# Optimization experiments

Measured on AMD Instinct MI355X. Metric: run time of the kernel, lower is better.

The kernel has to match this reference:

```python
import jax, jax.numpy as jnp
import numpy as np

NEG = 0.2  # LeakyReLU slope

def lrelu(x):
    return jnp.where(x >= 0, x, NEG * x)

def conv2d(x, w, pad):
    return jax.lax.conv_general_dilated(x, w, (1, 1), [(pad, pad), (pad, pad)],
                                        dimension_numbers=('NCHW', 'OIHW', 'NCHW'))

def maxpool2(x):
    return jax.lax.reduce_window(x, -jnp.inf, jax.lax.max, (1, 1, 2, 2), (1, 1, 2, 2), 'VALID')

def batchnorm(x, g, b, eps=1e-5):
    m = jnp.mean(x, axis=(0, 2, 3), keepdims=True)
    v = jnp.var(x, axis=(0, 2, 3), keepdims=True)
    return (x - m) / jnp.sqrt(v + eps) * g[None, :, None, None] + b[None, :, None, None]

def features(x, cw1, bg1, bb1, cw2, bg2, bb2, cw3, bg3, bb3, cw4, bg4, bb4):
    x = maxpool2(lrelu(batchnorm(conv2d(x, cw1, 1), bg1, bb1)))
    x = maxpool2(lrelu(batchnorm(conv2d(x, cw2, 1), bg2, bb2)))
    x = lrelu(batchnorm(conv2d(x, cw3, 1), bg3, bb3))
    x = lrelu(batchnorm(conv2d(x, cw4, 1), bg4, bb4))
    return x  # [B,64,16,16]

def mhsa(x, wq, bq, wk, bk, wv, bv, rel_h, rel_w, ln_g, ln_b, heads=4):
    B, C, W, H = x.shape
    d, hw = C // heads, W * H
    def proj(w, b):
        return (jnp.einsum('oc,bchw->bohw', w, x) + b[None, :, None, None]).reshape(B, heads, d, hw)
    q, k, v = proj(wq, bq), proj(wk, bk), proj(wv, bv)
    cc = jnp.einsum('bhdi,bhdj->bhij', q, k)                 # content-content
    pos = (rel_h + rel_w).reshape(heads, d, hw)              # relative position bias
    cp = jnp.einsum('hdi,bhdj->bhij', pos, q)                # content-position
    attn = jax.nn.softmax(cc + cp, axis=-1)
    out = jnp.einsum('bhdj,bhij->bhdi', v, attn).reshape(B, C, W, H)
    m = jnp.mean(out, axis=(1, 2, 3), keepdims=True)
    va = jnp.var(out, axis=(1, 2, 3), keepdims=True)
    out = (out - m) / jnp.sqrt(va + 1e-5) * ln_g[None] + ln_b[None]
    return out + x

def cbam(x, cw1, cb1, cw2, cb2, sw, sb):
    avg, mx = jnp.mean(x, axis=(2, 3)), jnp.max(x, axis=(2, 3))
    def exc(f):
        return jnp.einsum('oc,bc->bo', cw2, jax.nn.relu(jnp.einsum('oc,bc->bo', cw1, f) + cb1)) + cb2
    x = jax.nn.sigmoid(exc(avg) + exc(mx))[:, :, None, None] * x
    sf = jnp.stack([jnp.mean(x, axis=1), jnp.max(x, axis=1)], axis=1)  # [B,2,H,W]
    sa = jax.nn.sigmoid(conv2d(sf, sw, 3) + sb[None, :, None, None])
    return sa * x

def sa_module(x, mh, cb):
    return mhsa(x, *mh) + cbam(x, *cb) + x

def setup_inputs() -> dict:
    key = jax.random.key(0)
    ks = jax.random.split(key, 24)
    rn = lambda k, s, sc=1.0: jax.random.normal(k, s, dtype=jnp.float32) * sc
    inp = {
        'input1': rn(ks[0], (64, 1, 64, 64)),
        'input2': rn(ks[1], (5, 5, 1, 64, 64)),
        'conv1_w': rn(ks[2], (64, 1, 3, 3), 0.3),
        'bn1_g': jnp.ones(64), 'bn1_b': jnp.zeros(64),
        'conv2_w': rn(ks[3], (64, 64, 3, 3), 0.05),
        'bn2_g': jnp.ones(64), 'bn2_b': jnp.zeros(64),
        'conv3_w': rn(ks[4], (64, 64, 3, 3), 0.05),
        'bn3_g': jnp.ones(64), 'bn3_b': jnp.zeros(64),
        'conv4_w': rn(ks[5], (64, 64, 3, 3), 0.05),
        'bn4_g': jnp.ones(64), 'bn4_b': jnp.zeros(64),
        'wq': rn(ks[6], (64, 64), 0.12), 'bq': rn(ks[7], (64,), 0.01),
        'wk': rn(ks[8], (64, 64), 0.12), 'bk': rn(ks[9], (64,), 0.01),
        'wv': rn(ks[10], (64, 64), 0.12), 'bv': rn(ks[11], (64,), 0.01),
        'rel_h': rn(ks[12], (1, 4, 16, 1, 16)),
        'rel_w': rn(ks[13], (1, 4, 16, 16, 1)),
        'ln_g': jnp.ones((64, 16, 16)), 'ln_b': jnp.zeros((64, 16, 16)),
        'ca_w1': rn(ks[14], (4, 64), 0.15), 'ca_b1': jnp.zeros(4),
        'ca_w2': rn(ks[15], (64, 4), 0.15), 'ca_b2': jnp.zeros(64),
        'sa_w': rn(ks[16], (1, 2, 7, 7), 0.1), 'sa_b': jnp.zeros(1),
        'cls_w': rn(ks[17], (256,), 0.05),
    }
    return inp

def reference(input1, input2, conv1_w, bn1_g, bn1_b, conv2_w, bn2_g, bn2_b,
              conv3_w, bn3_g, bn3_b, conv4_w, bn4_g, bn4_b,
              wq, bq, wk, bk, wv, bv, rel_h, rel_w, ln_g, ln_b,
              ca_w1, ca_b1, ca_w2, ca_b2, sa_w, sa_b, cls_w):
    fa = (conv1_w, bn1_g, bn1_b, conv2_w, bn2_g, bn2_b, conv3_w, bn3_g, bn3_b, conv4_w, bn4_g, bn4_b)
    mh = (wq, bq, wk, bk, wv, bv, rel_h, rel_w, ln_g, ln_b)
    cb = (ca_w1, ca_b1, ca_w2, ca_b2, sa_w, sa_b)
    q = sa_module(features(input1, *fa), mh, cb)                      # [B,64,16,16]
    S = jax.vmap(lambda imgs: sa_module(features(imgs, *fa), mh, cb))(input2)  # [ncls,shot,64,16,16]
    ncls, shot = input2.shape[0], input2.shape[1]
    B, C, Hh, Ww = q.shape
    hw = Hh * Ww
    # per-class covariance over channels (CovaBlock.cal_covariance)
    X = S.transpose(0, 2, 1, 3, 4).reshape(ncls, C, shot * hw)
    Xc = X - jnp.mean(X, axis=2, keepdims=True)
    cov = jnp.einsum('ncm,ndm->ncd', Xc, Xc) / (hw * shot - 1)        # [ncls,C,C]
    # query similarity: diag(q^T Cov q) done as fused quadratic form
    Q = q.reshape(B, C, hw)
    Qn = Q / jnp.linalg.norm(Q, axis=2, keepdims=True)
    sim = jnp.einsum('bci,jcd,bdi->bji', Qn, cov, Qn)                 # [B,ncls,hw]
    # classifier: LeakyReLU -> Dropout(eval=identity) -> Conv1d(k=hw, stride=hw, no bias)
    out = jnp.einsum('bjk,k->bj', lrelu(sim), cls_w)
    return out
```

## Files before the change

kernel.cpp:

```cpp
#include <hip/hip_runtime.h>
#include <hip/hip_bf16.h>

__device__ __forceinline__ float lrelu(float x){ return x >= 0.f ? x : 0.2f*x; }
__device__ __forceinline__ float sigm(float x){ return 1.f/(1.f+__expf(-x)); }

typedef short short8 __attribute__((ext_vector_type(8)));
typedef float f32x16 __attribute__((ext_vector_type(16)));

static constexpr size_t OFF_X0    = 0;
static constexpr size_t OFF_POS   = 475712;
static constexpr size_t OFF_WQT   = 492096;
static constexpr size_t OFF_STATS = 504384;
static constexpr size_t OFF_P1    = 507456;
static constexpr size_t OFF_P2    = 6340160;
static constexpr size_t OFF_RES   = 10714688;
static constexpr size_t OFF_MU    = 12172864;
static constexpr size_t OFF_COV   = 12173184;
static constexpr size_t OFF_SIM   = 12193664;
static constexpr size_t OFF_R1    = 12275584;
static constexpr size_t OFF_C2    = OFF_R1;
static constexpr size_t OFF_ATP   = OFF_R1;
static constexpr size_t OFF_C3    = OFF_R1 + 5832704;
static constexpr size_t OFF_C4    = OFF_R1 + 8749056;
static constexpr size_t OFF_CKV   = OFF_R1 + 10207232;
static constexpr size_t OFF_MHRAW = OFF_R1 + 14581760;
static constexpr size_t OFF_QN    = OFF_R1 + 17543680;
static constexpr size_t OFF_WH    = OFF_R1 + 21737984;
static constexpr size_t OFF_WL    = OFF_WH + 18432;

__device__ __forceinline__ int bn_group(int img){ return (img < 64) ? 0 : (1 + (img-64)/5); }

__device__ __forceinline__ void bn_ab(const float* __restrict__ sums, int g, int c, float n,
                                      float gw, float bw, float& a, float& b)
{
    const float sum = sums[(g*64+c)*2], ss = sums[(g*64+c)*2+1];
    const float m = sum/n;
    const float var = fmaxf(ss/n - m*m, 0.f);
    const float istd = 1.f/sqrtf(var + 1e-5f);
    a = gw*istd;
    b = bw - m*a;
}

__global__ __launch_bounds__(256) void prep_k(const float* __restrict__ in1, const float* __restrict__ in2,
        const float* __restrict__ relh, const float* __restrict__ relw,
        const float* __restrict__ wq, const float* __restrict__ wk, const float* __restrict__ wv,
        const float* __restrict__ cw2,
        float* __restrict__ ws)
{
    int idx = blockIdx.x*256 + threadIdx.x;
    if (idx < 364544) { ws[OFF_X0+idx] = (idx < 262144 ? in1[idx] : in2[idx-262144]); return; }
    idx -= 364544;
    if (idx < 16384) {
        const int h = idx>>12, r = idx&4095, i = r>>4, d = r&15;
        ws[OFF_POS+idx] = relh[h*256 + d*16 + (i&15)] + relw[h*256 + d*16 + (i>>4)];
        return;
    }
    idx -= 16384;
    if (idx < 12288) {
        const int s = idx/4096, r = idx%4096, c = r>>6, o = r&63;
        const float* wp = (s==0)?wq:((s==1)?wk:wv);
        ws[OFF_WQT+idx] = wp[o*64 + c];
        return;
    }
    idx -= 12288;
    if (idx < 3072) { ws[OFF_STATS+idx] = 0.f; return; }
    idx -= 3072;
    if (idx < 20480) { ws[OFF_COV+idx] = 0.f; return; }
    idx -= 20480;
    if (idx < 36864) {
        const int och = idx/576, r = idx%576, cin = r/9, k9 = r%9;
        const float v = cw2[idx];
        __hip_bfloat16 hb = __float2bfloat16(v);
        const float hv = __bfloat162float(hb);
        __hip_bfloat16 lb = __float2bfloat16(v - hv);
        unsigned short* WH = (unsigned short*)(ws + OFF_WH);
        unsigned short* WL = (unsigned short*)(ws + OFF_WL);
        const int d = k9*4096 + och*64 + cin;
        WH[d] = *(unsigned short*)&hb;
        WL[d] = *(unsigned short*)&lb;
    }
}

template<int H, int W, int CIN, int CH, int OCB, int PT, bool STORE, bool INBN>
__global__ __launch_bounds__(256) void conv3x3_k(const float* __restrict__ in,
                                                 const float* __restrict__ wt,
                                                 float* __restrict__ out,
                                                 float* __restrict__ bnsum,
                                                 const float* __restrict__ isums,
                                                 const float* __restrict__ igw,
                                                 const float* __restrict__ ibw,
                                                 int ihw)
{
    constexpr int P = W + 1;
    constexpr int PLANE = H * P;
    constexpr int HW = H * W;
    constexpr int PASSES = HW / (256 * PT);
    constexpr int NLD = CH * HW / 256;
    __shared__ float lds[CH * PLANE];
    __shared__ float redS[OCB*4], redQ[OCB*4];
    __shared__ float abA[64], abB[64];
    const int img = blockIdx.x;
    const int och0 = blockIdx.y * OCB;
    const int t = threadIdx.x;

    if constexpr (INBN) {
        if (t < CIN) {
            const int gi = bn_group(img);
            const float nin = (float)(((gi==0)?64:5) * ihw);
            float a, b;
            bn_ab(isums, gi, t, nin, igw[t], ibw[t], a, b);
            abA[t]=a; abB[t]=b;
        }
        __syncthreads();
    }

    float acc[PASSES][OCB][PT];
#pragma unroll
    for (int a=0;a<PASSES;a++)
#pragma unroll
      for (int o=0;o<OCB;o++)
#pragma unroll
        for (int p=0;p<PT;p++) acc[a][o][p]=0.f;

    for (int idx = t; idx < CH*HW; idx += 256) {
        const int c = idx / HW, p = idx % HW;
        float v = in[((size_t)img*CIN + c)*HW + p];
        if constexpr (INBN) v = lrelu(abA[c]*v + abB[c]);
        lds[c*PLANE + (p/W)*P + (p%W)] = v;
    }
    __syncthreads();

    for (int cc0 = 0; cc0 < CIN; cc0 += CH) {
        float pre[(CIN > CH) ? NLD : 1];
        if constexpr (CIN > CH) {
            if (cc0 + CH < CIN) {
#pragma unroll
                for (int j=0;j<NLD;j++){
                    const int idx = j*256 + t;
                    const int c = idx / HW, p = idx % HW;
                    pre[j] = in[((size_t)img*CIN + cc0 + CH + c)*HW + p];
                }
            }
        }
        for (int c = 0; c < CH; ++c) {
            float wr[OCB][9];
#pragma unroll
            for (int o=0;o<OCB;o++)
#pragma unroll
              for (int k=0;k<9;k++)
                wr[o][k] = wt[((size_t)(och0+o)*CIN + (cc0+c))*9 + k];
            const float* Lc = lds + c*PLANE;
#pragma unroll
            for (int ps=0; ps<PASSES; ++ps) {
                const int px0 = (ps*256 + t)*PT;
                const int y = px0 / W, x0 = px0 % W;
#pragma unroll
                for (int ky=0; ky<3; ++ky) {
                    const int yy = y + ky - 1;
                    if (yy >= 0 && yy < H) {
                        const float* Lr = Lc + yy*P;
                        float r[PT+2];
                        r[0] = (x0 > 0) ? Lr[x0-1] : 0.f;
#pragma unroll
                        for (int k2=0;k2<PT;k2++) r[k2+1] = Lr[x0+k2];
                        r[PT+1] = (x0+PT < W) ? Lr[x0+PT] : 0.f;
#pragma unroll
                        for (int p=0;p<PT;p++)
#pragma unroll
                          for (int kx=0;kx<3;kx++) {
                              const float v = r[p+kx];
#pragma unroll
                              for (int o=0;o<OCB;o++)
                                  acc[ps][o][p] += v * wr[o][ky*3+kx];
                          }
                    }
                }
            }
        }
        if constexpr (CIN > CH) {
            if (cc0 + CH < CIN) {
                __syncthreads();
#pragma unroll
                for (int j=0;j<NLD;j++){
                    const int idx = j*256 + t;
                    const int c = idx / HW, p = idx % HW;
                    float v = pre[j];
                    if constexpr (INBN) v = lrelu(abA[cc0+CH+c]*v + abB[cc0+CH+c]);
                    lds[c*PLANE + (p/W)*P + (p%W)] = v;
                }
                __syncthreads();
            }
        }
    }
    if constexpr (STORE) {
#pragma unroll
        for (int ps=0; ps<PASSES; ++ps) {
            const int px0 = (ps*256 + t)*PT;
#pragma unroll
            for (int o=0;o<OCB;o++)
#pragma unroll
              for (int p=0;p<PT;p++)
                out[((size_t)img*64 + och0+o)*HW + px0 + p] = acc[ps][o][p];
        }
    }
    const int g = bn_group(img);
    const int wv = t >> 6;
#pragma unroll
    for (int o=0;o<OCB;o++){
        float s=0.f, ss=0.f;
#pragma unroll
        for (int ps=0;ps<PASSES;ps++)
#pragma unroll
          for (int p=0;p<PT;p++){ const float v=acc[ps][o][p]; s+=v; ss+=v*v; }
#pragma unroll
        for (int off=32; off>0; off>>=1){ s += __shfl_xor(s, off); ss += __shfl_xor(ss, off); }
        if ((t&63)==0){ redS[o*4+wv]=s; redQ[o*4+wv]=ss; }
    }
    __syncthreads();
    if (t < OCB*2){
        const int o = t>>1, metric = t&1;
        const float v = metric ? (redQ[o*4]+redQ[o*4+1]+redQ[o*4+2]+redQ[o*4+3])
                               : (redS[o*4]+redS[o*4+1]+redS[o*4+2]+redS[o*4+3]);
        atomicAdd(&bnsum[(g*64 + och0+o)*2 + metric], v);
    }
}

__global__ __launch_bounds__(256) void conv2mfma_k(const float* __restrict__ p1,
        const unsigned short* __restrict__ whi, const unsigned short* __restrict__ wlo,
        float* __restrict__ c2)
{
    __shared__ __align__(16) unsigned short Bx[6*34*72];
    const int img = blockIdx.x, rowblk = blockIdx.y;
    const int t = threadIdx.x;

    for (int i=t; i<6*2*72; i+=256){
        const int ly = i/144, r2 = i%144, xs = r2/72, c = r2%72;
        Bx[(ly*34 + xs*33)*72 + c] = 0;
    }
    unsigned int lo_pack[24];
    const int y0 = rowblk*4 - 1;
    {
        int it = 0;
        for (int lin=t; lin<12288; lin+=256, ++it){
            const int c = lin/192, r = lin%192, ly = r>>5, x = r&31;
            const int y = y0 + ly;
            float v = 0.f;
            if (y>=0 && y<32) v = p1[((size_t)img*64 + c)*1024 + y*32 + x];
            __hip_bfloat16 hb = __float2bfloat16(v);
            const float hv = __bfloat162float(hb);
            __hip_bfloat16 lb = __float2bfloat16(v - hv);
            Bx[(ly*34 + x + 1)*72 + c] = *(unsigned short*)&hb;
            const unsigned int lu = *(unsigned short*)&lb;
            if (it & 1) lo_pack[it>>1] |= (lu<<16); else lo_pack[it>>1] = lu;
        }
    }
    __syncthreads();

    const int lane = t & 63, wv = t >> 6;
    const int mt = wv & 1, ntp = wv >> 1;
    const int m = lane & 31, kg = lane >> 5;
    const int nt0 = ntp*2, nt1 = nt0 + 1;

    f32x16 acc0, acc1;
#pragma unroll
    for (int r=0;r<16;r++){ acc0[r]=0.f; acc1[r]=0.f; }

    for (int ky=0; ky<3; ky++){
      for (int kx=0; kx<3; kx++){
        const int s = ky*3 + kx;
        const unsigned short* wh = whi + ((s*64 + mt*32 + m)<<6) + kg*8;
        const unsigned short* wl = wlo + ((s*64 + mt*32 + m)<<6) + kg*8;
        const int b0 = ((nt0+ky)*34 + m + kx)*72 + kg*8;
        const int b1 = ((nt1+ky)*34 + m + kx)*72 + kg*8;
        short8 ah[4], al[4], bh0[4], bh1[4];
#pragma unroll
        for (int ch=0; ch<4; ch++){
            ah[ch]  = *(const short8*)(wh + ch*16);
            al[ch]  = *(const short8*)(wl + ch*16);
            bh0[ch] = *(const short8*)(Bx + b0 + ch*16);
            bh1[ch] = *(const short8*)(Bx + b1 + ch*16);
        }
#pragma unroll
        for (int ch=0; ch<4; ch++){
            acc0 = __builtin_amdgcn_mfma_f32_32x32x16_bf16(ah[ch], bh0[ch], acc0, 0,0,0);
            acc1 = __builtin_amdgcn_mfma_f32_32x32x16_bf16(ah[ch], bh1[ch], acc1, 0,0,0);
        }
#pragma unroll
        for (int ch=0; ch<4; ch++){
            acc0 = __builtin_amdgcn_mfma_f32_32x32x16_bf16(al[ch], bh0[ch], acc0, 0,0,0);
            acc1 = __builtin_amdgcn_mfma_f32_32x32x16_bf16(al[ch], bh1[ch], acc1, 0,0,0);
        }
      }
    }
    __syncthreads();
    {
        int it = 0;
        for (int lin=t; lin<12288; lin+=256, ++it){
            const int c = lin/192, r = lin%192, ly = r>>5, x = r&31;
            const unsigned int lu = (it&1) ? (lo_pack[it>>1]>>16) : (lo_pack[it>>1]&0xffffu);
            Bx[(ly*34 + x + 1)*72 + c] = (unsigned short)lu;
        }
    }
    __syncthreads();
    for (int ky=0; ky<3; ky++){
      for (int kx=0; kx<3; kx++){
        const int s = ky*3 + kx;
        const unsigned short* wh = whi + ((s*64 + mt*32 + m)<<6) + kg*8;
        const int b0 = ((nt0+ky)*34 + m + kx)*72 + kg*8;
        const int b1 = ((nt1+ky)*34 + m + kx)*72 + kg*8;
#pragma unroll
        for (int ch=0; ch<4; ch++){
            const short8 ah  = *(const short8*)(wh + ch*16);
            const short8 bl0 = *(const short8*)(Bx + b0 + ch*16);
            const short8 bl1 = *(const short8*)(Bx + b1 + ch*16);
            acc0 = __builtin_amdgcn_mfma_f32_32x32x16_bf16(ah, bl0, acc0, 0,0,0);
            acc1 = __builtin_amdgcn_mfma_f32_32x32x16_bf16(ah, bl1, acc1, 0,0,0);
        }
      }
    }
    const int px0 = (rowblk*4 + nt0)*32 + m;
    const int px1 = (rowblk*4 + nt1)*32 + m;
#pragma unroll
    for (int r=0; r<16; r++){
        const int och = mt*32 + (r&3) + 8*(r>>2) + 4*kg;
        c2[((size_t)img*64 + och)*1024 + px0] = acc0[r];
        c2[((size_t)img*64 + och)*1024 + px1] = acc1[r];
    }
}

__global__ __launch_bounds__(256) void bnstats2_k(const float* __restrict__ in, float* __restrict__ sums)
{
    __shared__ float rs[4], rq[4];
    const int img = blockIdx.x, c = blockIdx.y, t = threadIdx.x;
    const float4 v = ((const float4*)(in + ((size_t)img*64 + c)*1024))[t];
    float s = v.x+v.y+v.z+v.w;
    float q = v.x*v.x+v.y*v.y+v.z*v.z+v.w*v.w;
#pragma unroll
    for (int off=32; off>0; off>>=1){ s += __shfl_xor(s, off); q += __shfl_xor(q, off); }
    if ((t&63)==0){ rs[t>>6]=s; rq[t>>6]=q; }
    __syncthreads();
    if (t==0){
        const int g = bn_group(img);
        atomicAdd(&sums[(g*64+c)*2],   rs[0]+rs[1]+rs[2]+rs[3]);
        atomicAdd(&sums[(g*64+c)*2+1], rq[0]+rq[1]+rq[2]+rq[3]);
    }
}

__global__ __launch_bounds__(256) void bnpoolconv1_k(const float* __restrict__ x0,
        const float* __restrict__ cw, const float* __restrict__ sums,
        const float* __restrict__ gw, const float* __restrict__ bw,
        float* __restrict__ out)
{
    __shared__ float xl[64*65];
    const int img = blockIdx.x, och = blockIdx.y, t = threadIdx.x;
    const float* xp = x0 + (size_t)img*4096;
    for (int idx=t; idx<4096; idx+=256) xl[(idx>>6)*65 + (idx&63)] = xp[idx];
    float w[9];
#pragma unroll
    for (int k=0;k<9;k++) w[k] = cw[och*9+k];
    const int g = bn_group(img);
    const float n = (float)(((g==0)?64:5) * 4096);
    float a, b;
    bn_ab(sums, g, och, n, gw[och], bw[och], a, b);
    __syncthreads();
    const int oy = t>>3, ox0 = (t&7)*4;
    float r[4][10];
#pragma unroll
    for (int rr=0; rr<4; ++rr){
        const int yy = 2*oy-1+rr;
#pragma unroll
        for (int cc=0; cc<10; ++cc){
            const int xx = 2*ox0-1+cc;
            r[rr][cc] = (yy>=0 && yy<64 && xx>=0 && xx<64) ? xl[yy*65+xx] : 0.f;
        }
    }
    float4 res;
    float* rp = (float*)&res;
#pragma unroll
    for (int p=0;p<4;p++){
        float best = -1e30f;
#pragma unroll
        for (int sy=0; sy<2; ++sy)
#pragma unroll
          for (int sx=0; sx<2; ++sx){
            float s=0.f;
#pragma unroll
            for (int ky=0;ky<3;ky++)
#pragma unroll
              for (int kx=0;kx<3;kx++)
                s += r[sy+ky][2*p+sx+kx]*w[ky*3+kx];
            best = fmaxf(best, lrelu(a*s+b));
          }
        rp[p] = best;
    }
    *(float4*)(out + ((size_t)img*64+och)*1024 + oy*32 + ox0) = res;
}

template<int H, int W>
__global__ __launch_bounds__(256) void bnpool_k(const float* __restrict__ in, const float* __restrict__ sums,
                                 const float* __restrict__ gw, const float* __restrict__ bw,
                                 float* __restrict__ out)
{
    const int img = blockIdx.x, c = blockIdx.y, t = threadIdx.x;
    const int g = bn_group(img);
    const float n = (float)(((g==0)?64:5) * H * W);
    float a, b;
    bn_ab(sums, g, c, n, gw[c], bw[c], a, b);
    constexpr int W2=W/2, HW=H*W, N2=(H/2)*W2;
    const float* pl = in + ((size_t)img*64 + c)*HW;
    float* po = out + ((size_t)img*64 + c)*N2;
    for (int opx=t; opx<N2; opx+=256) {
        const int oy=opx/W2, ox=opx%W2;
        const float* q = pl + (2*oy)*W + 2*ox;
        const float v0=lrelu(a*q[0]+b), v1=lrelu(a*q[1]+b), v2=lrelu(a*q[W]+b), v3=lrelu(a*q[W+1]+b);
        po[opx] = fmaxf(fmaxf(v0,v1),fmaxf(v2,v3));
    }
}

__global__ __launch_bounds__(256) void proj_k(const float* __restrict__ c4, const float* __restrict__ wT,
               const float* __restrict__ bq, const float* __restrict__ bk, const float* __restrict__ bv,
               const float* __restrict__ sums4, const float* __restrict__ gw4, const float* __restrict__ bw4,
               float* __restrict__ ckv)
{
    __shared__ float xl[64*256];
    const int img = blockIdx.x, s = blockIdx.y, t = threadIdx.x;
    const int gi = bn_group(img);
    const float nin = (float)(((gi==0)?64:5) * 256);
    {
        const float4* in4 = (const float4*)(c4 + (size_t)img*16384);
        float4* xl4 = (float4*)xl;
        for (int i=t; i<4096; i+=256){
            float4 v = in4[i];
            const int c = i>>6;
            float a, b;
            bn_ab(sums4, gi, c, nin, gw4[c], bw4[c], a, b);
            v.x=lrelu(a*v.x+b); v.y=lrelu(a*v.y+b); v.z=lrelu(a*v.z+b); v.w=lrelu(a*v.w+b);
            xl4[i] = v;
        }
    }
    const float* bias = (s==0)?bq:((s==1)?bk:bv);
    const int sofs = (s==0)?16:((s==1)?0:32);
    const float* wp = wT + s*4096;
    const int o0 = (t>>4)*4, i0 = (t&15)*16;
    const int h = o0>>4, d0 = o0&15;
    __syncthreads();
    float acc[4][16];
    float b0[4];
#pragma unroll
    for (int o=0;o<4;o++) b0[o]=bias[o0+o];
#pragma unroll
    for (int o=0;o<4;o++)
#pragma unroll
      for (int i=0;i<16;i++) acc[o][i]=b0[o];
    for (int c=0;c<64;c++){
        const float4 w4 = *(const float4*)(wp + c*64 + o0);
        const float* xr = xl + c*256 + i0;
#pragma unroll
        for (int k=0;k<4;k++){
            const float4 x4 = *(const float4*)(xr + 4*k);
            acc[0][4*k+0]+=w4.x*x4.x; acc[0][4*k+1]+=w4.x*x4.y; acc[0][4*k+2]+=w4.x*x4.z; acc[0][4*k+3]+=w4.x*x4.w;
            acc[1][4*k+0]+=w4.y*x4.x; acc[1][4*k+1]+=w4.y*x4.y; acc[1][4*k+2]+=w4.y*x4.z; acc[1][4*k+3]+=w4.y*x4.w;
            acc[2][4*k+0]+=w4.z*x4.x; acc[2][4*k+1]+=w4.z*x4.y; acc[2][4*k+2]+=w4.z*x4.z; acc[2][4*k+3]+=w4.z*x4.w;
            acc[3][4*k+0]+=w4.w*x4.x; acc[3][4*k+1]+=w4.w*x4.y; acc[3][4*k+2]+=w4.w*x4.z; acc[3][4*k+3]+=w4.w*x4.w;
        }
    }
#pragma unroll
    for (int ii=0;ii<16;ii++){
        const float4 v = make_float4(acc[0][ii],acc[1][ii],acc[2][ii],acc[3][ii]);
        *(float4*)(ckv + (((size_t)img*4 + h)*256 + i0+ii)*48 + sofs + d0) = v;
    }
}

__global__ __launch_bounds__(256) void attnp_k(const float* __restrict__ ckv, const float* __restrict__ pos,
                               float* __restrict__ part)
{
    const int img = blockIdx.x, h = blockIdx.y, jc = blockIdx.z, i = threadIdx.x;
    const size_t jb = (((size_t)img*4 + h)*256)*48;
    float areg[32];
    {
        const float* myrow = ckv + jb + (size_t)i*48;
#pragma unroll
        for (int k=0;k<4;k++) *(float4*)&areg[4*k]    = *(const float4*)(myrow + 16 + 4*k);
#pragma unroll
        for (int k=0;k<4;k++) *(float4*)&areg[16+4*k] = *(const float4*)(pos + h*4096 + i*16 + 4*k);
    }
    float mrun = -1e30f, l = 0.f;
    float accv[16];
#pragma unroll
    for (int d=0;d<16;d++) accv[d]=0.f;

    const int jend = jc*64 + 64;
    for (int j0=jc*64; j0<jend; j0+=2){
        const float* r0 = ckv + jb + (size_t)j0*48;
        const float* r1 = r0 + 48;
        float s0a=0.f, s0b=0.f, s1a=0.f, s1b=0.f;
#pragma unroll
        for (int dd=0; dd<16; ++dd){
            s0a += areg[2*dd]  *r0[2*dd];
            s0b += areg[2*dd+1]*r0[2*dd+1];
            s1a += areg[2*dd]  *r1[2*dd];
            s1b += areg[2*dd+1]*r1[2*dd+1];
        }
        const float s0 = s0a+s0b, s1 = s1a+s1b;
        const float mnew = fmaxf(mrun, fmaxf(s0,s1));
        const float al = __expf(mrun - mnew);
        const float e0 = __expf(s0 - mnew), e1 = __expf(s1 - mnew);
        mrun = mnew;
        l = l*al + e0 + e1;
        const float* v0 = r0 + 32;
        const float* v1 = r1 + 32;
#pragma unroll
        for (int d=0;d<16;d++) accv[d] = accv[d]*al + e0*v0[d] + e1*v1[d];
    }
    float* pp = part + ((((size_t)img*4 + h)*4 + jc)*18)*256;
    pp[i]       = mrun;
    pp[256 + i] = l;
#pragma unroll
    for (int d=0;d<16;d++) pp[(2+d)*256 + i] = accv[d];
}

__global__ __launch_bounds__(256) void attnm_k(const float* __restrict__ part, float* __restrict__ mhraw)
{
    const int img = blockIdx.x, h = blockIdx.y, i = threadIdx.x;
    const float* pb = part + (((size_t)img*4 + h)*4*18)*256;
    float mc[4], lc[4];
#pragma unroll
    for (int c=0;c<4;c++){ mc[c] = pb[c*4608 + i]; lc[c] = pb[c*4608 + 256 + i]; }
    const float ms = fmaxf(fmaxf(mc[0],mc[1]), fmaxf(mc[2],mc[3]));
    float wgt[4]; float ls = 0.f;
#pragma unroll
    for (int c=0;c<4;c++){ wgt[c] = __expf(mc[c]-ms); ls += wgt[c]*lc[c]; }
    const float rl = 1.f/ls;
#pragma unroll
    for (int d=0;d<16;d++){
        float v = 0.f;
#pragma unroll
        for (int c=0;c<4;c++) v += wgt[c]*pb[c*4608 + (2+d)*256 + i];
        mhraw[((size_t)img*64 + h*16 + d)*256 + i] = v*rl;
    }
}

__global__ __launch_bounds__(256) void post_k(const float* __restrict__ mhraw,
        const float* __restrict__ lng, const float* __restrict__ lnb,
        const float* __restrict__ c4,
        const float* __restrict__ sums4, const float* __restrict__ gw4, const float* __restrict__ bw4,
        const float* __restrict__ w1, const float* __restrict__ b1,
        const float* __restrict__ w2, const float* __restrict__ b2,
        const float* __restrict__ sw, const float* __restrict__ sb,
        float* __restrict__ res)
{
    __shared__ float r1[256], r2[256];
    __shared__ float favg[64], fmx[64], z1s[8], ca[64];
    __shared__ float sf[512];
    __shared__ float wl[98];
    __shared__ float mh_s[2];
    __shared__ float aA[64], aB[64];
    __shared__ float sa_l[256];
    const int img = blockIdx.x, t = threadIdx.x;
    const float* mb  = mhraw + (size_t)img*16384;
    const float* fbr = c4    + (size_t)img*16384;

    if (t<64){
        const int gi = bn_group(img);
        const float nin = (float)(((gi==0)?64:5) * 256);
        float a, b;
        bn_ab(sums4, gi, t, nin, gw4[t], bw4[t], a, b);
        aA[t]=a; aB[t]=b;
    }
    if (t<98) wl[t] = sw[t];

    {
        const float4* mb4 = (const float4*)mb;
        float s=0.f, ss=0.f;
        for (int i=t; i<4096; i+=256){
            const float4 v = mb4[i];
            s  += v.x+v.y+v.z+v.w;
            ss += v.x*v.x+v.y*v.y+v.z*v.z+v.w*v.w;
        }
        r1[t]=s; r2[t]=ss; __syncthreads();
        for (int st=128;st>0;st>>=1){ if(t<st){r1[t]+=r1[t+st]; r2[t]+=r2[t+st];} __syncthreads(); }
        if (t==0){
            const float m = r1[0]/16384.f;
            const float var = fmaxf(r2[0]/16384.f - m*m, 0.f);
            mh_s[0]=m; mh_s[1]=1.f/sqrtf(var+1e-5f);
        }
    }
    {
        const int c = t>>2, part = t&3;
        const float a = aA[c], b = aB[c];
        const float4* p4 = (const float4*)(fbr + c*256 + part*64);
        float s=0.f, mx=-1e30f;
        for (int k=0;k<16;k++){
            const float4 v = p4[k];
            const float f0=lrelu(a*v.x+b), f1=lrelu(a*v.y+b), f2=lrelu(a*v.z+b), f3=lrelu(a*v.w+b);
            s += f0+f1+f2+f3;
            mx = fmaxf(mx, fmaxf(fmaxf(f0,f1),fmaxf(f2,f3)));
        }
        __syncthreads();
        r1[t]=s; r2[t]=mx;
        __syncthreads();
        if (t<64){
            favg[t] = (r1[t*4]+r1[t*4+1]+r1[t*4+2]+r1[t*4+3])/256.f;
            fmx[t]  = fmaxf(fmaxf(r2[t*4],r2[t*4+1]),fmaxf(r2[t*4+2],r2[t*4+3]));
        }
    }
    __syncthreads();
    if (t<8){
        const int which = t>>2, o = t&3;
        const float* f = which? fmx : favg;
        float z = b1[o];
        for (int c=0;c<64;c++) z += w1[o*64+c]*f[c];
        z1s[t] = fmaxf(z, 0.f);
    }
    __syncthreads();
    if (t<64){
        float z = 2.f*b2[t];
#pragma unroll
        for (int k=0;k<4;k++) z += w2[t*4+k]*(z1s[k]+z1s[4+k]);
        ca[t] = sigm(z);
    }
    __syncthreads();
    {
        float s=0.f, mx=-1e30f;
        for (int c=0;c<64;c++){
            const float fv = lrelu(aA[c]*fbr[c*256+t] + aB[c]);
            const float v = ca[c]*fv;
            s += v; mx = fmaxf(mx, v);
        }
        sf[t]     = s/64.f;
        sf[256+t] = mx;
    }
    __syncthreads();
    {
        float sacc = sb[0];
        const int y = t>>4, x = t&15;
        for (int ch=0; ch<2; ++ch)
          for (int ky=0; ky<7; ++ky){
            const int yy = y+ky-3;
            if (yy<0||yy>=16) continue;
            for (int kx=0; kx<7; ++kx){
                const int xx = x+kx-3;
                if (xx<0||xx>=16) continue;
                sacc += sf[ch*256 + yy*16 + xx]*wl[ch*49 + ky*7 + kx];
            }
          }
        sa_l[t] = sigm(sacc);
    }
    __syncthreads();
    {
        const int q = t & 63;
        const int cb = t >> 6;
        const float m = mh_s[0], istd = mh_s[1];
        const float4* mb4 = (const float4*)mb;
        const float4* fb4 = (const float4*)fbr;
        const float4* lg4 = (const float4*)lng;
        const float4* lb4 = (const float4*)lnb;
        float4* res4 = (float4*)(res + (size_t)img*16384);
        const float sa0=sa_l[4*q], sa1=sa_l[4*q+1], sa2=sa_l[4*q+2], sa3=sa_l[4*q+3];
#pragma unroll 4
        for (int cc=0; cc<16; ++cc){
            const int c = cb*16 + cc;
            const int i4 = c*64 + q;
            const float4 mv = mb4[i4], fv = fb4[i4], gv = lg4[i4], bv = lb4[i4];
            const float a = aA[c], b = aB[c], cf = ca[c];
            float4 r;
            r.x = (mv.x-m)*istd*gv.x + bv.x + lrelu(a*fv.x+b)*(2.f + sa0*cf);
            r.y = (mv.y-m)*istd*gv.y + bv.y + lrelu(a*fv.y+b)*(2.f + sa1*cf);
            r.z = (mv.z-m)*istd*gv.z + bv.z + lrelu(a*fv.z+b)*(2.f + sa2*cf);
            r.w = (mv.w-m)*istd*gv.w + bv.w + lrelu(a*fv.w+b)*(2.f + sa3*cf);
            res4[i4] = r;
        }
    }
}

__global__ __launch_bounds__(256) void covmu_k(const float* __restrict__ res, float* __restrict__ mu)
{
    __shared__ float r1[256];
    const int n = blockIdx.x, c = blockIdx.y, t = threadIdx.x;
    float s=0.f;
    for (int sh=0; sh<5; ++sh)
        s += res[((size_t)(64 + n*5 + sh)*64 + c)*256 + t];
    r1[t]=s; __syncthreads();
    for (int st=128;st>0;st>>=1){ if(t<st) r1[t]+=r1[t+st]; __syncthreads(); }
    if (t==0) mu[n*64+c] = r1[0]/1280.f;
}

__global__ __launch_bounds__(256) void cov_k(const float* __restrict__ res, const float* __restrict__ mu,
                                             float* __restrict__ cov)
{
    __shared__ float Xl[64*129];
    const int n = blockIdx.x, by = blockIdx.y, sh = blockIdx.z, t = threadIdx.x;
    const int c = by*16 + (t>>4);
    const int d0 = (t&15)*4;
    float acc[4] = {0.f,0.f,0.f,0.f};
    for (int half=0; half<2; ++half){
        __syncthreads();
        for (int idx=t; idx<8192; idx+=256){
            const int ch = idx>>7, p = idx&127;
            Xl[ch*129+p] = res[((size_t)(64+n*5+sh)*64 + ch)*256 + half*128 + p] - mu[n*64+ch];
        }
        __syncthreads();
        for (int p=0;p<128;p++){
            const float xc = Xl[c*129+p];
#pragma unroll
            for (int k=0;k<4;k++) acc[k] += xc*Xl[(d0+k)*129+p];
        }
    }
#pragma unroll
    for (int k=0;k<4;k++) atomicAdd(&cov[((size_t)n*64 + c)*64 + d0+k], acc[k]*(1.f/1279.f));
}

__global__ __launch_bounds__(64) void qn_k(const float* __restrict__ res, float* __restrict__ qn)
{
    const int b = blockIdx.x, c = blockIdx.y, t = threadIdx.x;
    const size_t base = ((size_t)b*64 + c)*256;
    const float4 v = *(const float4*)(res + base + t*4);
    float ss = v.x*v.x + v.y*v.y + v.z*v.z + v.w*v.w;
#pragma unroll
    for (int off=32; off>0; off>>=1) ss += __shfl_xor(ss, off);
    const float inv = 1.f/sqrtf(ss);
    float4 o; o.x=v.x*inv; o.y=v.y*inv; o.z=v.z*inv; o.w=v.w*inv;
    *(float4*)(qn + base + t*4) = o;
}

__global__ __launch_bounds__(256) void sim_k(const float* __restrict__ qn, const float* __restrict__ cov,
                                             float* __restrict__ sim)
{
    __shared__ float covj[64*65];
    __shared__ float Vl[64*68];
    __shared__ float simred[320];
    const int b = blockIdx.x, iq = blockIdx.y, t = threadIdx.x;
    const int i0g = iq*64;
    for (int idx=t; idx<4096; idx+=256){
        const int c = idx>>6, il = idx&63;
        Vl[c*68+il] = qn[((size_t)b*64+c)*256 + i0g + il];
    }
    for (int idx=t; idx<320; idx+=256) simred[idx]=0.f;
    const int c0 = (t>>4)*4, i0 = (t&15)*4;
    for (int j=0;j<5;j++){
        __syncthreads();
        for (int idx=t; idx<4096; idx+=256)
            covj[(idx>>6)*65 + (idx&63)] = cov[(size_t)j*4096 + idx];
        __syncthreads();
        float pt[4][4];
#pragma unroll
        for (int a=0;a<4;a++)
#pragma unroll
          for (int bb=0;bb<4;bb++) pt[a][bb]=0.f;
        for (int d=0; d<64; ++d){
            const float4 vv = *(const float4*)&Vl[d*68 + i0];
            float cw[4];
#pragma unroll
            for (int cc=0;cc<4;cc++) cw[cc] = covj[(c0+cc)*65 + d];
#pragma unroll
            for (int cc=0;cc<4;cc++){
                pt[cc][0] += cw[cc]*vv.x;
                pt[cc][1] += cw[cc]*vv.y;
                pt[cc][2] += cw[cc]*vv.z;
                pt[cc][3] += cw[cc]*vv.w;
            }
        }
#pragma unroll
        for (int ii=0;ii<4;ii++){
            float s = 0.f;
#pragma unroll
            for (int cc=0;cc<4;cc++) s += pt[cc][ii]*Vl[(c0+cc)*68 + i0+ii];
            atomicAdd(&simred[j*64 + i0 + ii], s);
        }
    }
    __syncthreads();
    for (int idx=t; idx<320; idx+=256){
        const int j = idx>>6, il = idx&63;
        sim[((size_t)b*5 + j)*256 + i0g + il] = simred[idx];
    }
}

__global__ __launch_bounds__(256) void cls_k(const float* __restrict__ sim, const float* __restrict__ cw,
                                             float* __restrict__ out)
{
    __shared__ float red[256];
    const int b = blockIdx.x, t = threadIdx.x;
    const float w = cw[t];
    for (int j=0;j<5;j++){
        const float v = sim[((size_t)b*5 + j)*256 + t];
        red[t] = lrelu(v)*w;
        __syncthreads();
        for (int st=128;st>0;st>>=1){ if(t<st) red[t]+=red[t+st]; __syncthreads(); }
        if (t==0) out[b*5+j] = red[0];
        __syncthreads();
    }
}

extern "C" void kernel_launch(void* const* d_in, const int* in_sizes, int n_in,
                              void* d_out, int out_size, void* d_ws, size_t ws_size,
                              hipStream_t stream)
{
    const float* IN[31];
    for (int i=0;i<31;i++) IN[i] = (const float*)d_in[i];
    float* W = (float*)d_ws;
    float* OUT = (float*)d_out;
    const unsigned short* WHp = (const unsigned short*)(W + OFF_WH);
    const unsigned short* WLp = (const unsigned short*)(W + OFF_WL);

    prep_k<<<1772,256,0,stream>>>(IN[0],IN[1],IN[20],IN[21],IN[14],IN[16],IN[18],IN[5],W);

    conv3x3_k<64,64,1,1,4,4,false,false><<<dim3(89,16),256,0,stream>>>(W+OFF_X0, IN[2], nullptr, W+OFF_STATS, nullptr,nullptr,nullptr,0);
    bnpoolconv1_k<<<dim3(89,64),256,0,stream>>>(W+OFF_X0, IN[2], W+OFF_STATS, IN[3], IN[4], W+OFF_P1);

    conv2mfma_k<<<dim3(89,8),256,0,stream>>>(W+OFF_P1, WHp, WLp, W+OFF_C2);
    bnstats2_k<<<dim3(89,64),256,0,stream>>>(W+OFF_C2, W+OFF_STATS+768);
    bnpool_k<32,32><<<dim3(89,64),256,0,stream>>>(W+OFF_C2, W+OFF_STATS+768, IN[6], IN[7], W+OFF_P2);

    conv3x3_k<16,16,64,16,8,1,true,false><<<dim3(89,8),256,0,stream>>>(W+OFF_P2, IN[8], W+OFF_C3, W+OFF_STATS+1536, nullptr,nullptr,nullptr,0);

    conv3x3_k<16,16,64,16,8,1,true,true><<<dim3(89,8),256,0,stream>>>(W+OFF_C3, IN[11], W+OFF_C4, W+OFF_STATS+2304,
                                                                      W+OFF_STATS+1536, IN[9], IN[10], 256);

    proj_k<<<dim3(89,3),256,0,stream>>>(W+OFF_C4, W+OFF_WQT, IN[15], IN[17], IN[19],
                                        W+OFF_STATS+2304, IN[12], IN[13], W+OFF_CKV);
    attnp_k<<<dim3(89,4,4),256,0,stream>>>(W+OFF_CKV, W+OFF_POS, W+OFF_ATP);
    attnm_k<<<dim3(89,4),256,0,stream>>>(W+OFF_ATP, W+OFF_MHRAW);

    post_k<<<89,256,0,stream>>>(W+OFF_MHRAW, IN[22], IN[23], W+OFF_C4,
                                W+OFF_STATS+2304, IN[12], IN[13],
                                IN[24], IN[25], IN[26], IN[27], IN[28], IN[29], W+OFF_RES);

    covmu_k<<<dim3(5,64),256,0,stream>>>(W+OFF_RES, W+OFF_MU);
    cov_k<<<dim3(5,4,5),256,0,stream>>>(W+OFF_RES, W+OFF_MU, W+OFF_COV);
    qn_k<<<dim3(64,64),64,0,stream>>>(W+OFF_RES, W+OFF_QN);
    sim_k<<<dim3(64,4),256,0,stream>>>(W+OFF_QN, W+OFF_COV, W+OFF_SIM);
    cls_k<<<64,256,0,stream>>>(W+OFF_SIM, IN[30], OUT);
}
```

Before: 538.7 us.

## Pre-split conv2 input into padded bf16 hi/lo NHWC buffers, drop LDS staging

Adds a transpose kernel that converts the conv2 input once into padded channel-last bf16 hi and lo planes in global memory. The MFMA conv kernel then reads its B operands straight from global/L2 with no LDS staging, no in-kernel split and no second pass. Each block now handles two output rows, so the grid doubles. This trades an extra kernel launch and global round trip for removing the serialized LDS fill and the per-block hi/lo conversion, and it reads neighbour rows redundantly from cache.

```diff
diff --git a/kernel.cpp b/kernel.cpp
--- a/kernel.cpp
+++ b/kernel.cpp
@@ -23,6 +23,8 @@
 static constexpr size_t OFF_C3    = OFF_R1 + 5832704;
 static constexpr size_t OFF_C4    = OFF_R1 + 8749056;
 static constexpr size_t OFF_CKV   = OFF_R1 + 10207232;
+static constexpr size_t OFF_P1H   = OFF_CKV;
+static constexpr size_t OFF_P1L   = OFF_CKV + 3098624;
 static constexpr size_t OFF_MHRAW = OFF_R1 + 14581760;
 static constexpr size_t OFF_QN    = OFF_R1 + 17543680;
 static constexpr size_t OFF_WH    = OFF_R1 + 21737984;
@@ -225,106 +227,108 @@
     }
 }
 
-__global__ __launch_bounds__(256) void conv2mfma_k(const float* __restrict__ p1,
+__global__ __launch_bounds__(256) void t12_k(const float* __restrict__ p1,
+        unsigned short* __restrict__ p1h, unsigned short* __restrict__ p1l)
+{
+    __shared__ float Xl[64*129];
+    const int img = blockIdx.x, pb = blockIdx.y;
+    const int t = threadIdx.x;
+    const int px0 = pb*128;
+#pragma unroll 4
+    for (int it=0; it<32; ++it){
+        const int lin = it*256 + t;
+        const int c = lin >> 7, px = lin & 127;
+        Xl[c*129 + px] = p1[(size_t)img*65536 + c*1024 + px0 + px];
+    }
+    __syncthreads();
+    const size_t ob = (size_t)img*69632;
+#pragma unroll 4
+    for (int it=0; it<32; ++it){
+        const int lin = it*256 + t;
+        const int c = lin & 63, px = lin >> 6;
+        const float v = Xl[c*129 + px];
+        __hip_bfloat16 hb = __float2bfloat16(v);
+        const float hv = __bfloat162float(hb);
+        __hip_bfloat16 lb = __float2bfloat16(v - hv);
+        const int gpx = px0 + px;
+        const int y = gpx >> 5, x = gpx & 31;
+        const size_t o = ob + (size_t)y*2176 + (size_t)(x+1)*64 + c;
+        p1h[o] = *(unsigned short*)&hb;
+        p1l[o] = *(unsigned short*)&lb;
+    }
+    for (int i=t; i<512; i+=256){
+        const int r = i >> 7, half = (i>>6)&1, c = i & 63;
+        const int y = pb*4 + r;
+        const size_t o = ob + (size_t)y*2176 + (half ? 33*64 : 0) + c;
+        p1h[o] = 0; p1l[o] = 0;
+    }
+}
+
+__global__ __launch_bounds__(256) void conv2mfma_k(const unsigned short* __restrict__ p1h,
+        const unsigned short* __restrict__ p1l,
         const unsigned short* __restrict__ whi, const unsigned short* __restrict__ wlo,
         float* __restrict__ c2)
 {
-    __shared__ __align__(16) unsigned short Bx[6*34*72];
     const int img = blockIdx.x, rowblk = blockIdx.y;
     const int t = threadIdx.x;
-
-    for (int i=t; i<6*2*72; i+=256){
-        const int ly = i/144, r2 = i%144, xs = r2/72, c = r2%72;
-        Bx[(ly*34 + xs*33)*72 + c] = 0;
-    }
-    unsigned int lo_pack[24];
-    const int y0 = rowblk*4 - 1;
-    {
-        int it = 0;
-        for (int lin=t; lin<12288; lin+=256, ++it){
-            const int c = lin/192, r = lin%192, ly = r>>5, x = r&31;
-            const int y = y0 + ly;
-            float v = 0.f;
-            if (y>=0 && y<32) v = p1[((size_t)img*64 + c)*1024 + y*32 + x];
-            __hip_bfloat16 hb = __float2bfloat16(v);
-            const float hv = __bfloat162float(hb);
-            __hip_bfloat16 lb = __float2bfloat16(v - hv);
-            Bx[(ly*34 + x + 1)*72 + c] = *(unsigned short*)&hb;
-            const unsigned int lu = *(unsigned short*)&lb;
-            if (it & 1) lo_pack[it>>1] |= (lu<<16); else lo_pack[it>>1] = lu;
-        }
-    }
-    __syncthreads();
-
     const int lane = t & 63, wv = t >> 6;
-    const int mt = wv & 1, ntp = wv >> 1;
+    const int mt = wv & 1, nt = wv >> 1;
     const int m = lane & 31, kg = lane >> 5;
-    const int nt0 = ntp*2, nt1 = nt0 + 1;
-
-    f32x16 acc0, acc1;
-#pragma unroll
-    for (int r=0;r<16;r++){ acc0[r]=0.f; acc1[r]=0.f; }
+
+    f32x16 acc;
+#pragma unroll
+    for (int r=0;r<16;r++) acc[r]=0.f;
+    short8 zz;
+#pragma unroll
+    for (int q=0;q<8;q++) zz[q]=0;
+
+    const int yout = rowblk*2 + nt;
+    const size_t ibase = (size_t)img*69632;
+    const unsigned short* wbh = whi + ((mt*32 + m)<<6) + kg*8;
+    const unsigned short* wbl = wlo + ((mt*32 + m)<<6) + kg*8;
 
     for (int ky=0; ky<3; ky++){
-      for (int kx=0; kx<3; kx++){
-        const int s = ky*3 + kx;
-        const unsigned short* wh = whi + ((s*64 + mt*32 + m)<<6) + kg*8;
-        const unsigned short* wl = wlo + ((s*64 + mt*32 + m)<<6) + kg*8;
-        const int b0 = ((nt0+ky)*34 + m + kx)*72 + kg*8;
-        const int b1 = ((nt1+ky)*34 + m + kx)*72 + kg*8;
-        short8 ah[4], al[4], bh0[4], bh1[4];
-#pragma unroll
-        for (int ch=0; ch<4; ch++){
-            ah[ch]  = *(const short8*)(wh + ch*16);
-            al[ch]  = *(const short8*)(wl + ch*16);
-            bh0[ch] = *(const short8*)(Bx + b0 + ch*16);
-            bh1[ch] = *(const short8*)(Bx + b1 + ch*16);
-        }
-#pragma unroll
-        for (int ch=0; ch<4; ch++){
-            acc0 = __builtin_amdgcn_mfma_f32_32x32x16_bf16(ah[ch], bh0[ch], acc0, 0,0,0);
-            acc1 = __builtin_amdgcn_mfma_f32_32x32x16_bf16(ah[ch], bh1[ch], acc1, 0,0,0);
-        }
-#pragma unroll
-        for (int ch=0; ch<4; ch++){
-            acc0 = __builtin_amdgcn_mfma_f32_32x32x16_bf16(al[ch], bh0[ch], acc0, 0,0,0);
-            acc1 = __builtin_amdgcn_mfma_f32_32x32x16_bf16(al[ch], bh1[ch], acc1, 0,0,0);
-        }
-      }
-    }
-    __syncthreads();
-    {
-        int it = 0;
-        for (int lin=t; lin<12288; lin+=256, ++it){
-            const int c = lin/192, r = lin%192, ly = r>>5, x = r&31;
-            const unsigned int lu = (it&1) ? (lo_pack[it>>1]>>16) : (lo_pack[it>>1]&0xffffu);
-            Bx[(ly*34 + x + 1)*72 + c] = (unsigned short)lu;
-        }
-    }
-    __syncthreads();
-    for (int ky=0; ky<3; ky++){
-      for (int kx=0; kx<3; kx++){
-        const int s = ky*3 + kx;
-        const unsigned short* wh = whi + ((s*64 + mt*32 + m)<<6) + kg*8;
-        const int b0 = ((nt0+ky)*34 + m + kx)*72 + kg*8;
-        const int b1 = ((nt1+ky)*34 + m + kx)*72 + kg*8;
-#pragma unroll
-        for (int ch=0; ch<4; ch++){
-            const short8 ah  = *(const short8*)(wh + ch*16);
-            const short8 bl0 = *(const short8*)(Bx + b0 + ch*16);
-            const short8 bl1 = *(const short8*)(Bx + b1 + ch*16);
-            acc0 = __builtin_amdgcn_mfma_f32_32x32x16_bf16(ah, bl0, acc0, 0,0,0);
-            acc1 = __builtin_amdgcn_mfma_f32_32x32x16_bf16(ah, bl1, acc1, 0,0,0);
-        }
-      }
-    }
-    const int px0 = (rowblk*4 + nt0)*32 + m;
-    const int px1 = (rowblk*4 + nt1)*32 + m;
+        const int y = yout + ky - 1;
+        const bool yok = (y>=0) && (y<32);
+        const unsigned short* rowh = p1h + ibase + (size_t)y*2176;
+        const unsigned short* rowl = p1l + ibase + (size_t)y*2176;
+        for (int kx=0; kx<3; kx++){
+            const int s = ky*3+kx;
+            const unsigned short* wh = wbh + (s<<12);
+            const unsigned short* wl = wbl + (s<<12);
+            const int bo = (m+kx)*64 + kg*8;
+            short8 ah[4], al[4], bh[4], bl[4];
+#pragma unroll
+            for (int ch=0; ch<4; ch++){
+                ah[ch] = *(const short8*)(wh + ch*16);
+                al[ch] = *(const short8*)(wl + ch*16);
+            }
+            if (yok){
+#pragma unroll
+                for (int ch=0; ch<4; ch++){
+                    bh[ch] = *(const short8*)(rowh + bo + ch*16);
+                    bl[ch] = *(const short8*)(rowl + bo + ch*16);
+                }
+            } else {
+#pragma unroll
+                for (int ch=0; ch<4; ch++){ bh[ch] = zz; bl[ch] = zz; }
+            }
+#pragma unroll
+            for (int ch=0; ch<4; ch++)
+                acc = __builtin_amdgcn_mfma_f32_32x32x16_bf16(ah[ch], bh[ch], acc, 0,0,0);
+#pragma unroll
+            for (int ch=0; ch<4; ch++)
+                acc = __builtin_amdgcn_mfma_f32_32x32x16_bf16(al[ch], bh[ch], acc, 0,0,0);
+#pragma unroll
+            for (int ch=0; ch<4; ch++)
+                acc = __builtin_amdgcn_mfma_f32_32x32x16_bf16(ah[ch], bl[ch], acc, 0,0,0);
+        }
+    }
+    const int px = yout*32 + m;
 #pragma unroll
     for (int r=0; r<16; r++){
         const int och = mt*32 + (r&3) + 8*(r>>2) + 4*kg;
-        c2[((size_t)img*64 + och)*1024 + px0] = acc0[r];
-        c2[((size_t)img*64 + och)*1024 + px1] = acc1[r];
+        c2[((size_t)img*64 + och)*1024 + px] = acc[r];
     }
 }
 
@@ -801,13 +805,16 @@
     float* OUT = (float*)d_out;
     const unsigned short* WHp = (const unsigned short*)(W + OFF_WH);
     const unsigned short* WLp = (const unsigned short*)(W + OFF_WL);
+    unsigned short* P1Hp = (unsigned short*)(W + OFF_P1H);
+    unsigned short* P1Lp = (unsigned short*)(W + OFF_P1L);
 
     prep_k<<<1772,256,0,stream>>>(IN[0],IN[1],IN[20],IN[21],IN[14],IN[16],IN[18],IN[5],W);
 
     conv3x3_k<64,64,1,1,4,4,false,false><<<dim3(89,16),256,0,stream>>>(W+OFF_X0, IN[2], nullptr, W+OFF_STATS, nullptr,nullptr,nullptr,0);
     bnpoolconv1_k<<<dim3(89,64),256,0,stream>>>(W+OFF_X0, IN[2], W+OFF_STATS, IN[3], IN[4], W+OFF_P1);
 
-    conv2mfma_k<<<dim3(89,8),256,0,stream>>>(W+OFF_P1, WHp, WLp, W+OFF_C2);
+    t12_k<<<dim3(89,8),256,0,stream>>>(W+OFF_P1, P1Hp, P1Lp);
+    conv2mfma_k<<<dim3(89,16),256,0,stream>>>(P1Hp, P1Lp, WHp, WLp, W+OFF_C2);
     bnstats2_k<<<dim3(89,64),256,0,stream>>>(W+OFF_C2, W+OFF_STATS+768);
     bnpool_k<32,32><<<dim3(89,64),256,0,stream>>>(W+OFF_C2, W+OFF_STATS+768, IN[6], IN[7], W+OFF_P2);
 
```

Measured after the change: 583.0 us. +8.2%, slower.

## Pre-split conv2 input into padded channel-last bf16 hi/lo planes

Applied to the files above, without the earlier changes.

Adds a transpose kernel that converts the fp32 NCHW pool1 output into padded NHWC bf16 hi and lo arrays in workspace, with zeroed border columns. conv2mfma_k then fills its LDS tile with contiguous 32-bit copies instead of strided fp32 loads, per-element bf16 splitting and a register-packed lo buffer. This is meant to remove uncoalesced gathers and conversion work from the MFMA conv. It costs an extra launch plus one more write and read of the activation.

```diff
diff --git a/kernel.cpp b/kernel.cpp
--- a/kernel.cpp
+++ b/kernel.cpp
@@ -23,6 +23,8 @@
 static constexpr size_t OFF_C3    = OFF_R1 + 5832704;
 static constexpr size_t OFF_C4    = OFF_R1 + 8749056;
 static constexpr size_t OFF_CKV   = OFF_R1 + 10207232;
+static constexpr size_t OFF_P1H   = OFF_CKV;
+static constexpr size_t OFF_P1L   = OFF_CKV + 3098624;
 static constexpr size_t OFF_MHRAW = OFF_R1 + 14581760;
 static constexpr size_t OFF_QN    = OFF_R1 + 17543680;
 static constexpr size_t OFF_WH    = OFF_R1 + 21737984;
@@ -225,33 +227,68 @@
     }
 }
 
-__global__ __launch_bounds__(256) void conv2mfma_k(const float* __restrict__ p1,
+__global__ __launch_bounds__(256) void t12_k(const float* __restrict__ p1,
+        unsigned short* __restrict__ p1h, unsigned short* __restrict__ p1l)
+{
+    __shared__ float Xl[64*129];
+    const int img = blockIdx.x, pb = blockIdx.y;
+    const int t = threadIdx.x;
+    const int px0 = pb*128;
+#pragma unroll 4
+    for (int it=0; it<32; ++it){
+        const int lin = it*256 + t;
+        const int c = lin >> 7, px = lin & 127;
+        Xl[c*129 + px] = p1[(size_t)img*65536 + c*1024 + px0 + px];
+    }
+    __syncthreads();
+    const size_t ob = (size_t)img*69632;
+#pragma unroll 4
+    for (int it=0; it<32; ++it){
+        const int lin = it*256 + t;
+        const int c = lin & 63, px = lin >> 6;
+        const float v = Xl[c*129 + px];
+        __hip_bfloat16 hb = __float2bfloat16(v);
+        const float hv = __bfloat162float(hb);
+        __hip_bfloat16 lb = __float2bfloat16(v - hv);
+        const int gpx = px0 + px;
+        const int y = gpx >> 5, x = gpx & 31;
+        const size_t o = ob + (size_t)y*2176 + (size_t)(x+1)*64 + c;
+        p1h[o] = *(unsigned short*)&hb;
+        p1l[o] = *(unsigned short*)&lb;
+    }
+    for (int i=t; i<512; i+=256){
+        const int r = i >> 7, half = (i>>6)&1, c = i & 63;
+        const int y = pb*4 + r;
+        const size_t o = ob + (size_t)y*2176 + (half ? 33*64 : 0) + c;
+        p1h[o] = 0; p1l[o] = 0;
+    }
+}
+
+__global__ __launch_bounds__(256) void conv2mfma_k(const unsigned short* __restrict__ p1h,
+        const unsigned short* __restrict__ p1l,
         const unsigned short* __restrict__ whi, const unsigned short* __restrict__ wlo,
         float* __restrict__ c2)
 {
     __shared__ __align__(16) unsigned short Bx[6*34*72];
     const int img = blockIdx.x, rowblk = blockIdx.y;
     const int t = threadIdx.x;
-
-    for (int i=t; i<6*2*72; i+=256){
-        const int ly = i/144, r2 = i%144, xs = r2/72, c = r2%72;
-        Bx[(ly*34 + xs*33)*72 + c] = 0;
-    }
-    unsigned int lo_pack[24];
     const int y0 = rowblk*4 - 1;
-    {
-        int it = 0;
-        for (int lin=t; lin<12288; lin+=256, ++it){
-            const int c = lin/192, r = lin%192, ly = r>>5, x = r&31;
-            const int y = y0 + ly;
-            float v = 0.f;
-            if (y>=0 && y<32) v = p1[((size_t)img*64 + c)*1024 + y*32 + x];
-            __hip_bfloat16 hb = __float2bfloat16(v);
-            const float hv = __bfloat162float(hb);
-            __hip_bfloat16 lb = __float2bfloat16(v - hv);
-            Bx[(ly*34 + x + 1)*72 + c] = *(unsigned short*)&hb;
-            const unsigned int lu = *(unsigned short*)&lb;
-            if (it & 1) lo_pack[it>>1] |= (lu<<16); else lo_pack[it>>1] = lu;
+    const size_t ob = (size_t)img*69632;
+
+#pragma unroll
+    for (int ly=0; ly<6; ++ly){
+        const int y = y0 + ly;
+        if (y>=0 && y<32){
+            const unsigned int* s32 = (const unsigned int*)(p1h + ob + (size_t)y*2176);
+            for (int i=t; i<1088; i+=256){
+                const int px = i>>5, cv = i&31;
+                *(unsigned int*)&Bx[(ly*34+px)*72 + cv*2] = s32[i];
+            }
+        } else {
+            for (int i=t; i<1088; i+=256){
+                const int px = i>>5, cv = i&31;
+                *(unsigned int*)&Bx[(ly*34+px)*72 + cv*2] = 0u;
+            }
         }
     }
     __syncthreads();
@@ -293,12 +330,20 @@
       }
     }
     __syncthreads();
-    {
-        int it = 0;
-        for (int lin=t; lin<12288; lin+=256, ++it){
-            const int c = lin/192, r = lin%192, ly = r>>5, x = r&31;
-            const unsigned int lu = (it&1) ? (lo_pack[it>>1]>>16) : (lo_pack[it>>1]&0xffffu);
-            Bx[(ly*34 + x + 1)*72 + c] = (unsigned short)lu;
+#pragma unroll
+    for (int ly=0; ly<6; ++ly){
+        const int y = y0 + ly;
+        if (y>=0 && y<32){
+            const unsigned int* s32 = (const unsigned int*)(p1l + ob + (size_t)y*2176);
+            for (int i=t; i<1088; i+=256){
+                const int px = i>>5, cv = i&31;
+                *(unsigned int*)&Bx[(ly*34+px)*72 + cv*2] = s32[i];
+            }
+        } else {
+            for (int i=t; i<1088; i+=256){
+                const int px = i>>5, cv = i&31;
+                *(unsigned int*)&Bx[(ly*34+px)*72 + cv*2] = 0u;
+            }
         }
     }
     __syncthreads();
@@ -801,13 +846,16 @@
     float* OUT = (float*)d_out;
     const unsigned short* WHp = (const unsigned short*)(W + OFF_WH);
     const unsigned short* WLp = (const unsigned short*)(W + OFF_WL);
+    unsigned short* P1Hp = (unsigned short*)(W + OFF_P1H);
+    unsigned short* P1Lp = (unsigned short*)(W + OFF_P1L);
 
     prep_k<<<1772,256,0,stream>>>(IN[0],IN[1],IN[20],IN[21],IN[14],IN[16],IN[18],IN[5],W);
 
     conv3x3_k<64,64,1,1,4,4,false,false><<<dim3(89,16),256,0,stream>>>(W+OFF_X0, IN[2], nullptr, W+OFF_STATS, nullptr,nullptr,nullptr,0);
     bnpoolconv1_k<<<dim3(89,64),256,0,stream>>>(W+OFF_X0, IN[2], W+OFF_STATS, IN[3], IN[4], W+OFF_P1);
 
-    conv2mfma_k<<<dim3(89,8),256,0,stream>>>(W+OFF_P1, WHp, WLp, W+OFF_C2);
+    t12_k<<<dim3(89,8),256,0,stream>>>(W+OFF_P1, P1Hp, P1Lp);
+    conv2mfma_k<<<dim3(89,8),256,0,stream>>>(P1Hp, P1Lp, WHp, WLp, W+OFF_C2);
     bnstats2_k<<<dim3(89,64),256,0,stream>>>(W+OFF_C2, W+OFF_STATS+768);
     bnpool_k<32,32><<<dim3(89,64),256,0,stream>>>(W+OFF_C2, W+OFF_STATS+768, IN[6], IN[7], W+OFF_P2);
 
```

After: 541.8 us. About the same (+0.6%).
